# Kernel tuning notes

Hardware: AMD Instinct MI355X
Metric: run time of the kernel (lower is better)

The kernel has to match this reference:

```python
import jax, jax.numpy as jnp
import numpy as np

BN_EPS = 1e-5


def setup_inputs() -> dict:
    key = jax.random.key(0)
    ks = jax.random.split(key, 6)
    N, C, T, V = 64, 64, 300, 25
    num_A, O = 3, 64
    x = jax.random.normal(ks[0], (N, C, T, V), dtype=jnp.float32)
    A = jax.random.uniform(ks[1], (num_A, V, V), dtype=jnp.float32)
    # 1x1 conv weights per adjacency branch: W[a, o, c], bias b[a, o]
    W = jax.random.normal(ks[2], (num_A, O, C), dtype=jnp.float32) * (1.0 / np.sqrt(C))
    b = jax.random.normal(ks[3], (num_A, O), dtype=jnp.float32) * 0.01
    gamma = jnp.ones((O,), dtype=jnp.float32)
    beta = jnp.zeros((O,), dtype=jnp.float32)
    return {"x": x, "A": A, "W": W, "b": b, "gamma": gamma, "beta": beta}


def reference(x, A, W, b, gamma, beta):
    # x: [N, C, T, V]; A: [num_A, V, V]; W: [num_A, O, C]; b: [num_A, O]
    # For each branch a: xa = x @ A_a over the joint dim V, then a 1x1 conv
    # (channel mix W_a + bias b_a), accumulated over branches.
    z = jnp.einsum('nctv,avw->anctw', x, A)          # [num_A, N, C, T, V]
    y = jnp.einsum('anctw,aoc->notw', z, W)          # [N, O, T, V]
    y = y + jnp.sum(b, axis=0)[None, :, None, None]
    # BatchNorm2d (training mode: batch statistics over N, T, V per channel)
    mean = jnp.mean(y, axis=(0, 2, 3), keepdims=True)
    var = jnp.mean((y - mean) ** 2, axis=(0, 2, 3), keepdims=True)
    y = (y - mean) * jax.lax.rsqrt(var + BN_EPS)
    y = y * gamma[None, :, None, None] + beta[None, :, None, None]
    return jax.nn.relu(y)
```

## Files before the change

### kernel.cpp

```cpp
#include <hip/hip_runtime.h>


typedef __attribute__((ext_vector_type(8))) short short8;
typedef __attribute__((ext_vector_type(4))) float f32x4;

static __device__ __forceinline__ float bf2f(unsigned short u) {
    return __uint_as_float(((unsigned)u) << 16);
}
static __device__ __forceinline__ unsigned short f2bf(float f) {
    unsigned u = __float_as_uint(f);
    u += 0x7FFFu + ((u >> 16) & 1u);
    return (unsigned short)(u >> 16);
}

#define MFMA16(a, b, c) __builtin_amdgcn_mfma_f32_16x16x32_bf16((a), (b), (c), 0, 0, 0)

__global__ __launch_bounds__(256, 4)
void gcn_k1(const void* __restrict__ xg, const void* __restrict__ Ag,
            const void* __restrict__ Wg, const void* __restrict__ gammag,
            float* __restrict__ gstats, unsigned short* __restrict__ y_ws)
{
    const int tid  = threadIdx.x;
    const int wv   = tid >> 6;
    const int lane = tid & 63;
    const int n16  = lane & 15;
    const int kg   = lane >> 4;
    const int bx   = blockIdx.x;
    const int nb   = bx / 75;
    const int tile = bx - nb * 75;

    const bool isbf = (*(const unsigned*)gammag) == 0x3F803F80u;

    __shared__ __align__(16) unsigned short xs2[256 * 32];
    __shared__ __align__(16) unsigned short AsT[3 * 32 * 32];
    __shared__ __align__(16) unsigned short zsT[112 * 68];
    __shared__ float red[128];

    if (tid < 128) red[tid] = 0.f;

    short8 wfrag[3][2];
    #pragma unroll
    for (int a = 0; a < 3; ++a)
        #pragma unroll
        for (int k2 = 0; k2 < 2; ++k2) {
            const int off = (a * 64 + wv * 16 + n16) * 64 + k2 * 32 + kg * 8;
            if (isbf) {
                wfrag[a][k2] = *(const short8*)((const unsigned short*)Wg + off);
            } else {
                const float* wp = (const float*)Wg + off;
                const float4 w0 = *(const float4*)wp;
                const float4 w1 = *(const float4*)(wp + 4);
                short8 f;
                f[0] = (short)f2bf(w0.x); f[1] = (short)f2bf(w0.y);
                f[2] = (short)f2bf(w0.z); f[3] = (short)f2bf(w0.w);
                f[4] = (short)f2bf(w1.x); f[5] = (short)f2bf(w1.y);
                f[6] = (short)f2bf(w1.z); f[7] = (short)f2bf(w1.w);
                wfrag[a][k2] = f;
            }
        }

    for (int s = tid; s < 3072; s += 256) {
        const int a = s >> 10, w = (s >> 5) & 31, v = s & 31;
        unsigned short val = 0;
        if (v < 25 && w < 25) {
            const int src = (a * 25 + v) * 25 + w;
            val = isbf ? ((const unsigned short*)Ag)[src] : f2bf(((const float*)Ag)[src]);
        }
        AsT[s] = val;
    }

    {
        #pragma unroll
        for (int vv = 25; vv < 32; ++vv) xs2[tid * 32 + vv] = 0;
    }
    if (isbf) {
        const unsigned* xp = (const unsigned*)xg;
        for (int p = tid; p < 3200; p += 256) {
            const int c = p / 50, pc = p - c * 50;
            const unsigned u = xp[(nb * 64 + c) * 3750 + tile * 50 + pc];
            const int r0 = pc * 2, r1 = r0 + 1;
            const int dt0 = r0 / 25, v0 = r0 - dt0 * 25;
            const int dt1 = r1 / 25, v1 = r1 - dt1 * 25;
            xs2[(c * 4 + dt0) * 32 + v0] = (unsigned short)(u & 0xFFFFu);
            xs2[(c * 4 + dt1) * 32 + v1] = (unsigned short)(u >> 16);
        }
    } else {
        const float2* xp = (const float2*)xg;
        for (int p = tid; p < 3200; p += 256) {
            const int c = p / 50, pc = p - c * 50;
            const float2 f = xp[(nb * 64 + c) * 3750 + tile * 50 + pc];
            const int r0 = pc * 2, r1 = r0 + 1;
            const int dt0 = r0 / 25, v0 = r0 - dt0 * 25;
            const int dt1 = r1 / 25, v1 = r1 - dt1 * 25;
            xs2[(c * 4 + dt0) * 32 + v0] = f2bf(f.x);
            xs2[(c * 4 + dt1) * 32 + v1] = f2bf(f.y);
        }
    }

    __syncthreads();

    f32x4 acc[7];
    #pragma unroll
    for (int mt = 0; mt < 7; ++mt) acc[mt] = (f32x4){0.f, 0.f, 0.f, 0.f};

    const f32x4 zero4 = (f32x4){0.f, 0.f, 0.f, 0.f};

    #pragma unroll
    for (int a = 0; a < 3; ++a) {
        const short8 bA0 = *(const short8*)&AsT[(a * 32 +      n16) * 32 + kg * 8];
        const short8 bA1 = *(const short8*)&AsT[(a * 32 + 16 + n16) * 32 + kg * 8];
        f32x4 d[4][2];
        #pragma unroll
        for (int mt = 0; mt < 4; ++mt) {
            const short8 af = *(const short8*)&xs2[(wv * 64 + mt * 16 + n16) * 32 + kg * 8];
            d[mt][0] = MFMA16(af, bA0, zero4);
            d[mt][1] = MFMA16(af, bA1, zero4);
        }
        #pragma unroll
        for (int mt = 0; mt < 4; ++mt) {
            const int c = 16 * wv + mt * 4 + kg;
            #pragma unroll
            for (int r = 0; r < 4; ++r) {
                const int w0 = n16;
                zsT[(r * 25 + w0) * 68 + c] = f2bf(d[mt][0][r]);
                const int w1 = 16 + n16;
                if (w1 < 25) zsT[(r * 25 + w1) * 68 + c] = f2bf(d[mt][1][r]);
            }
        }
        __syncthreads();

        #pragma unroll
        for (int mt = 0; mt < 7; ++mt) {
            #pragma unroll
            for (int k2 = 0; k2 < 2; ++k2) {
                const unsigned short* zp = &zsT[(mt * 16 + n16) * 68 + k2 * 32 + kg * 8];
                const ushort4 z0 = *(const ushort4*)zp;
                const ushort4 z1 = *(const ushort4*)(zp + 4);
                short8 bf;
                bf[0] = (short)z0.x; bf[1] = (short)z0.y; bf[2] = (short)z0.z; bf[3] = (short)z0.w;
                bf[4] = (short)z1.x; bf[5] = (short)z1.y; bf[6] = (short)z1.z; bf[7] = (short)z1.w;
                acc[mt] = MFMA16(wfrag[a][k2], bf, acc[mt]);
            }
        }
        __syncthreads();
    }

    #pragma unroll
    for (int r = 0; r < 4; ++r) {
        const int o = 16 * wv + kg * 4 + r;
        const unsigned rowbase = (unsigned)(nb * 64 + o) * 7500u + (unsigned)tile * 100u;
        float s = 0.f, q = 0.f;
        #pragma unroll
        for (int mt = 0; mt < 7; ++mt) {
            const float v = acc[mt][r];
            const bool valid = (mt < 6) | (n16 < 4);
            const float vm = valid ? v : 0.f;
            s += vm; q += vm * vm;
            const float vhi = __shfl_xor(v, 1);
            if (((n16 & 1) == 0) && valid) {
                const unsigned idx = rowbase + (unsigned)(mt * 16 + n16);
                *(unsigned*)(y_ws + idx) = (unsigned)f2bf(v) | ((unsigned)f2bf(vhi) << 16);
            }
        }
        #pragma unroll
        for (int off = 1; off < 16; off <<= 1) {
            s += __shfl_xor(s, off);
            q += __shfl_xor(q, off);
        }
        if (n16 == 0) { atomicAdd(&red[o], s); atomicAdd(&red[64 + o], q); }
    }

    __syncthreads();
    if (tid < 128) atomicAdd(&gstats[tid], red[tid]);
}

__global__ __launch_bounds__(256)
void gcn_k2(const float* __restrict__ gstats, const unsigned* __restrict__ y32,
            const void* __restrict__ gammag, const void* __restrict__ betag,
            void* __restrict__ outg)
{
    __shared__ float sc[64], sh[64];
    const int tid = threadIdx.x;
    const bool isbf = (*(const unsigned*)gammag) == 0x3F803F80u;

    if (tid < 64) {
        const float inv  = 1.0f / 480000.0f;
        const float mean = gstats[tid] * inv;
        const float var  = gstats[64 + tid] * inv - mean * mean;
        const float rstd = rsqrtf(var + 1e-5f);
        float g, be;
        if (isbf) { g = bf2f(((const unsigned short*)gammag)[tid]); be = bf2f(((const unsigned short*)betag)[tid]); }
        else      { g = ((const float*)gammag)[tid];                be = ((const float*)betag)[tid]; }
        sc[tid] = g * rstd;
        sh[tid] = be - mean * g * rstd;
    }
    __syncthreads();

    const unsigned i = blockIdx.x * 256u + (unsigned)tid;
    const uint4 u = ((const uint4*)y32)[i];
    const unsigned b = i * 4u;
    unsigned wv[4] = {u.x, u.y, u.z, u.w};
    float res[8];
    #pragma unroll
    for (int j = 0; j < 4; ++j) {
        const unsigned o = ((b + j) / 3750u) & 63u;
        const float scl = sc[o], shf = sh[o];
        const float v0 = bf2f((unsigned short)(wv[j] & 0xFFFFu));
        const float v1 = bf2f((unsigned short)(wv[j] >> 16));
        res[2 * j]     = fmaxf(fmaf(v0, scl, shf), 0.f);
        res[2 * j + 1] = fmaxf(fmaf(v1, scl, shf), 0.f);
    }
    if (isbf) {
        uint4 outp;
        outp.x = (unsigned)f2bf(res[0]) | ((unsigned)f2bf(res[1]) << 16);
        outp.y = (unsigned)f2bf(res[2]) | ((unsigned)f2bf(res[3]) << 16);
        outp.z = (unsigned)f2bf(res[4]) | ((unsigned)f2bf(res[5]) << 16);
        outp.w = (unsigned)f2bf(res[6]) | ((unsigned)f2bf(res[7]) << 16);
        ((uint4*)outg)[i] = outp;
    } else {
        float4 f0 = make_float4(res[0], res[1], res[2], res[3]);
        float4 f1 = make_float4(res[4], res[5], res[6], res[7]);
        ((float4*)outg)[2 * i]     = f0;
        ((float4*)outg)[2 * i + 1] = f1;
    }
}

extern "C" void kernel_launch(void* const* d_in, const int* in_sizes, int n_in,
                              void* d_out, int out_size, void* d_ws, size_t ws_size,
                              hipStream_t stream)
{
    (void)in_sizes; (void)n_in; (void)out_size; (void)ws_size;
    const void* x     = d_in[0];
    const void* A     = d_in[1];
    const void* W     = d_in[2];
    const void* gamma = d_in[4];
    const void* beta  = d_in[5];

    float*          gstats = (float*)d_ws;
    unsigned short* y_ws   = (unsigned short*)d_ws + 256;

    hipMemsetAsync(d_ws, 0, 512, stream);
    gcn_k1<<<dim3(64 * 75), dim3(256), 0, stream>>>(x, A, W, gamma, gstats, y_ws);
    gcn_k2<<<dim3(15000), dim3(256), 0, stream>>>(gstats, (const unsigned*)y_ws, gamma, beta, d_out);
}
```

Before: 382.0 us.

## Recompute GEMMs in a second pass instead of storing intermediate y

Replaces the store-y-then-normalize scheme with a templated kernel run twice: the first pass computes only BatchNorm statistics, and the second recomputes the graph conv and channel mix and writes the normalized ReLU output directly. This removes the write and re-read of the bf16 intermediate tensor. In exchange x is read twice and all the MFMA work is done twice. Tiles grow to 12 timesteps per block, each wave keeps its z tile in its own swizzled LDS buffer with no block barriers, and W fragments are loaded per branch.

```diff
diff --git a/kernel.cpp b/kernel.cpp
--- a/kernel.cpp
+++ b/kernel.cpp
@@ -1,4 +1,5 @@
 #include <hip/hip_runtime.h>
+#include <hip/hip_bf16.h>
 
 
 typedef __attribute__((ext_vector_type(8))) short short8;
@@ -12,13 +13,27 @@
     u += 0x7FFFu + ((u >> 16) & 1u);
     return (unsigned short)(u >> 16);
 }
+static __device__ __forceinline__ unsigned pk2(float lo, float hi) {
+    return (unsigned)f2bf(lo) | ((unsigned)f2bf(hi) << 16);
+}
+static __device__ __forceinline__ short8 cvt8(float4 a, float4 b) {
+    short8 r;
+    r[0] = (short)f2bf(a.x); r[1] = (short)f2bf(a.y);
+    r[2] = (short)f2bf(a.z); r[3] = (short)f2bf(a.w);
+    r[4] = (short)f2bf(b.x); r[5] = (short)f2bf(b.y);
+    r[6] = (short)f2bf(b.z); r[7] = (short)f2bf(b.w);
+    return r;
+}
 
 #define MFMA16(a, b, c) __builtin_amdgcn_mfma_f32_16x16x32_bf16((a), (b), (c), 0, 0, 0)
-
-__global__ __launch_bounds__(256, 4)
-void gcn_k1(const void* __restrict__ xg, const void* __restrict__ Ag,
-            const void* __restrict__ Wg, const void* __restrict__ gammag,
-            float* __restrict__ gstats, unsigned short* __restrict__ y_ws)
+#define LDS_FENCE() __asm__ volatile("s_waitcnt lgkmcnt(0)" ::: "memory")
+
+template <bool STORE>
+__global__ __launch_bounds__(256, 2)
+void gcn_core(const void* __restrict__ xg, const void* __restrict__ Ag,
+              const void* __restrict__ Wg, const void* __restrict__ gammag,
+              const void* __restrict__ betag, float* __restrict__ gstats,
+              void* __restrict__ outg)
 {
     const int tid  = threadIdx.x;
     const int wv   = tid >> 6;
@@ -26,39 +41,63 @@
     const int n16  = lane & 15;
     const int kg   = lane >> 4;
     const int bx   = blockIdx.x;
-    const int nb   = bx / 75;
-    const int tile = bx - nb * 75;
+    const int nb   = bx / 25;
+    const int tile = bx - nb * 25;
+    const int t0   = tile * 12 + wv * 3;
 
     const bool isbf = (*(const unsigned*)gammag) == 0x3F803F80u;
 
-    __shared__ __align__(16) unsigned short xs2[256 * 32];
+    __shared__ __align__(16) unsigned short xls[768 * 32];
+    __shared__ __align__(16) unsigned short zbuf[4 * 2048];
     __shared__ __align__(16) unsigned short AsT[3 * 32 * 32];
-    __shared__ __align__(16) unsigned short zsT[112 * 68];
     __shared__ float red[128];
-
-    if (tid < 128) red[tid] = 0.f;
-
-    short8 wfrag[3][2];
-    #pragma unroll
-    for (int a = 0; a < 3; ++a)
-        #pragma unroll
-        for (int k2 = 0; k2 < 2; ++k2) {
-            const int off = (a * 64 + wv * 16 + n16) * 64 + k2 * 32 + kg * 8;
-            if (isbf) {
-                wfrag[a][k2] = *(const short8*)((const unsigned short*)Wg + off);
-            } else {
-                const float* wp = (const float*)Wg + off;
-                const float4 w0 = *(const float4*)wp;
-                const float4 w1 = *(const float4*)(wp + 4);
-                short8 f;
-                f[0] = (short)f2bf(w0.x); f[1] = (short)f2bf(w0.y);
-                f[2] = (short)f2bf(w0.z); f[3] = (short)f2bf(w0.w);
-                f[4] = (short)f2bf(w1.x); f[5] = (short)f2bf(w1.y);
-                f[6] = (short)f2bf(w1.z); f[7] = (short)f2bf(w1.w);
-                wfrag[a][k2] = f;
-            }
-        }
-
+    __shared__ float scsh[128];
+
+    if (!STORE) {
+        if (tid < 128) red[tid] = 0.f;
+    } else {
+        if (tid < 64) {
+            const float inv  = 1.0f / 480000.0f;
+            const float mean = gstats[tid] * inv;
+            const float var  = gstats[64 + tid] * inv - mean * mean;
+            const float rstd = rsqrtf(var + 1e-5f);
+            float g, be;
+            if (isbf) { g = bf2f(((const unsigned short*)gammag)[tid]); be = bf2f(((const unsigned short*)betag)[tid]); }
+            else      { g = ((const float*)gammag)[tid];                be = ((const float*)betag)[tid]; }
+            scsh[tid]      = g * rstd;
+            scsh[64 + tid] = be - mean * g * rstd;
+        }
+    }
+
+    for (int p = tid; p < 5376; p += 256) {
+        const int row = p / 7, v = 25 + (p - 7 * row);
+        xls[row * 32 + v] = 0;
+    }
+    if (isbf) {
+        const unsigned* xp = (const unsigned*)xg;
+        const unsigned cb = (unsigned)(nb * 64) * 3750u + (unsigned)tile * 150u;
+        for (int p = tid; p < 9600; p += 256) {
+            const int c = p / 150, r = p - 150 * c;
+            const unsigned u = xp[cb + (unsigned)c * 3750u + r];
+            const int e = 2 * r;
+            const int t1 = e / 25,      v1 = e - 25 * t1;
+            const int t2 = (e + 1) / 25, v2 = (e + 1) - 25 * t2;
+            xls[(t1 * 64 + c) * 32 + v1] = (unsigned short)(u & 0xFFFFu);
+            xls[(t2 * 64 + c) * 32 + v2] = (unsigned short)(u >> 16);
+        }
+    } else {
+        const float2* xp = (const float2*)xg;
+        const unsigned cb = (unsigned)(nb * 64) * 3750u + (unsigned)tile * 150u;
+        for (int p = tid; p < 9600; p += 256) {
+            const int c = p / 150, r = p - 150 * c;
+            const float2 f = xp[cb + (unsigned)c * 3750u + r];
+            const int e = 2 * r;
+            const int t1 = e / 25,      v1 = e - 25 * t1;
+            const int t2 = (e + 1) / 25, v2 = (e + 1) - 25 * t2;
+            xls[(t1 * 64 + c) * 32 + v1] = f2bf(f.x);
+            xls[(t2 * 64 + c) * 32 + v2] = f2bf(f.y);
+        }
+    }
     for (int s = tid; s < 3072; s += 256) {
         const int a = s >> 10, w = (s >> 5) & 31, v = s & 31;
         unsigned short val = 0;
@@ -69,159 +108,154 @@
         AsT[s] = val;
     }
 
-    {
-        #pragma unroll
-        for (int vv = 25; vv < 32; ++vv) xs2[tid * 32 + vv] = 0;
-    }
-    if (isbf) {
-        const unsigned* xp = (const unsigned*)xg;
-        for (int p = tid; p < 3200; p += 256) {
-            const int c = p / 50, pc = p - c * 50;
-            const unsigned u = xp[(nb * 64 + c) * 3750 + tile * 50 + pc];
-            const int r0 = pc * 2, r1 = r0 + 1;
-            const int dt0 = r0 / 25, v0 = r0 - dt0 * 25;
-            const int dt1 = r1 / 25, v1 = r1 - dt1 * 25;
-            xs2[(c * 4 + dt0) * 32 + v0] = (unsigned short)(u & 0xFFFFu);
-            xs2[(c * 4 + dt1) * 32 + v1] = (unsigned short)(u >> 16);
-        }
-    } else {
-        const float2* xp = (const float2*)xg;
-        for (int p = tid; p < 3200; p += 256) {
-            const int c = p / 50, pc = p - c * 50;
-            const float2 f = xp[(nb * 64 + c) * 3750 + tile * 50 + pc];
-            const int r0 = pc * 2, r1 = r0 + 1;
-            const int dt0 = r0 / 25, v0 = r0 - dt0 * 25;
-            const int dt1 = r1 / 25, v1 = r1 - dt1 * 25;
-            xs2[(c * 4 + dt0) * 32 + v0] = f2bf(f.x);
-            xs2[(c * 4 + dt1) * 32 + v1] = f2bf(f.y);
-        }
-    }
-
     __syncthreads();
 
-    f32x4 acc[7];
+    short8 xf[3][4];
     #pragma unroll
-    for (int mt = 0; mt < 7; ++mt) acc[mt] = (f32x4){0.f, 0.f, 0.f, 0.f};
+    for (int dt = 0; dt < 3; ++dt)
+        #pragma unroll
+        for (int ct = 0; ct < 4; ++ct)
+            xf[dt][ct] = *(const short8*)&xls[((wv * 3 + dt) * 64 + 16 * ct + n16) * 32 + 8 * kg];
+
+    f32x4 acc[3][2][4];
+    #pragma unroll
+    for (int dt = 0; dt < 3; ++dt)
+        #pragma unroll
+        for (int wt = 0; wt < 2; ++wt)
+            #pragma unroll
+            for (int ot = 0; ot < 4; ++ot)
+                acc[dt][wt][ot] = (f32x4){0.f, 0.f, 0.f, 0.f};
 
     const f32x4 zero4 = (f32x4){0.f, 0.f, 0.f, 0.f};
+    unsigned short* zb = &zbuf[wv * 2048];
+    const int swz = n16 & 7;
 
     #pragma unroll
     for (int a = 0; a < 3; ++a) {
-        const short8 bA0 = *(const short8*)&AsT[(a * 32 +      n16) * 32 + kg * 8];
-        const short8 bA1 = *(const short8*)&AsT[(a * 32 + 16 + n16) * 32 + kg * 8];
-        f32x4 d[4][2];
-        #pragma unroll
-        for (int mt = 0; mt < 4; ++mt) {
-            const short8 af = *(const short8*)&xs2[(wv * 64 + mt * 16 + n16) * 32 + kg * 8];
-            d[mt][0] = MFMA16(af, bA0, zero4);
-            d[mt][1] = MFMA16(af, bA1, zero4);
-        }
-        #pragma unroll
-        for (int mt = 0; mt < 4; ++mt) {
-            const int c = 16 * wv + mt * 4 + kg;
-            #pragma unroll
-            for (int r = 0; r < 4; ++r) {
-                const int w0 = n16;
-                zsT[(r * 25 + w0) * 68 + c] = f2bf(d[mt][0][r]);
-                const int w1 = 16 + n16;
-                if (w1 < 25) zsT[(r * 25 + w1) * 68 + c] = f2bf(d[mt][1][r]);
+        short8 wf[4][2];
+        #pragma unroll
+        for (int ot = 0; ot < 4; ++ot)
+            #pragma unroll
+            for (int h = 0; h < 2; ++h) {
+                const int off = ((a * 64 + 16 * ot + n16) * 64 + 32 * h + 8 * kg);
+                if (isbf) {
+                    wf[ot][h] = *(const short8*)((const unsigned short*)Wg + off);
+                } else {
+                    const float* wp = (const float*)Wg + off;
+                    wf[ot][h] = cvt8(*(const float4*)wp, *(const float4*)(wp + 4));
+                }
+            }
+        const short8 af0 = *(const short8*)&AsT[(a * 32 +      n16) * 32 + 8 * kg];
+        const short8 af1 = *(const short8*)&AsT[(a * 32 + 16 + n16) * 32 + 8 * kg];
+
+        #pragma unroll
+        for (int dt = 0; dt < 3; ++dt) {
+            LDS_FENCE();
+            #pragma unroll
+            for (int ct = 0; ct < 4; ++ct) {
+                const f32x4 d0 = MFMA16(xf[dt][ct], af0, zero4);
+                const f32x4 d1 = MFMA16(xf[dt][ct], af1, zero4);
+                const int gp = (2 * ct + (kg >> 1)) ^ swz;
+                const int so = gp * 8 + (kg & 1) * 4;
+                {   unsigned* p = (unsigned*)(zb + n16 * 64 + so);
+                    p[0] = pk2(d0[0], d0[1]); p[1] = pk2(d0[2], d0[3]); }
+                {   unsigned* p = (unsigned*)(zb + (16 + n16) * 64 + so);
+                    p[0] = pk2(d1[0], d1[1]); p[1] = pk2(d1[2], d1[3]); }
+            }
+            LDS_FENCE();
+            #pragma unroll
+            for (int wt = 0; wt < 2; ++wt)
+                #pragma unroll
+                for (int h = 0; h < 2; ++h) {
+                    const int gp = (4 * h + kg) ^ swz;
+                    const short8 zf = *(const short8*)(zb + (16 * wt + n16) * 64 + gp * 8);
+                    #pragma unroll
+                    for (int ot = 0; ot < 4; ++ot)
+                        acc[dt][wt][ot] = MFMA16(zf, wf[ot][h], acc[dt][wt][ot]);
+                }
+        }
+    }
+
+    if (!STORE) {
+        float s[4], q[4];
+        #pragma unroll
+        for (int ot = 0; ot < 4; ++ot) { s[ot] = 0.f; q[ot] = 0.f; }
+        #pragma unroll
+        for (int dt = 0; dt < 3; ++dt)
+            #pragma unroll
+            for (int wt = 0; wt < 2; ++wt)
+                #pragma unroll
+                for (int ot = 0; ot < 4; ++ot)
+                    #pragma unroll
+                    for (int r = 0; r < 4; ++r) {
+                        const float v = acc[dt][wt][ot][r];
+                        s[ot] += v; q[ot] += v * v;
+                    }
+        #pragma unroll
+        for (int ot = 0; ot < 4; ++ot) {
+            s[ot] += __shfl_xor(s[ot], 16); s[ot] += __shfl_xor(s[ot], 32);
+            q[ot] += __shfl_xor(q[ot], 16); q[ot] += __shfl_xor(q[ot], 32);
+        }
+        if (kg == 0) {
+            #pragma unroll
+            for (int ot = 0; ot < 4; ++ot) {
+                atomicAdd(&red[16 * ot + n16], s[ot]);
+                atomicAdd(&red[64 + 16 * ot + n16], q[ot]);
             }
         }
         __syncthreads();
-
-        #pragma unroll
-        for (int mt = 0; mt < 7; ++mt) {
-            #pragma unroll
-            for (int k2 = 0; k2 < 2; ++k2) {
-                const unsigned short* zp = &zsT[(mt * 16 + n16) * 68 + k2 * 32 + kg * 8];
-                const ushort4 z0 = *(const ushort4*)zp;
-                const ushort4 z1 = *(const ushort4*)(zp + 4);
-                short8 bf;
-                bf[0] = (short)z0.x; bf[1] = (short)z0.y; bf[2] = (short)z0.z; bf[3] = (short)z0.w;
-                bf[4] = (short)z1.x; bf[5] = (short)z1.y; bf[6] = (short)z1.z; bf[7] = (short)z1.w;
-                acc[mt] = MFMA16(wfrag[a][k2], bf, acc[mt]);
-            }
-        }
-        __syncthreads();
-    }
-
-    #pragma unroll
-    for (int r = 0; r < 4; ++r) {
-        const int o = 16 * wv + kg * 4 + r;
-        const unsigned rowbase = (unsigned)(nb * 64 + o) * 7500u + (unsigned)tile * 100u;
-        float s = 0.f, q = 0.f;
-        #pragma unroll
-        for (int mt = 0; mt < 7; ++mt) {
-            const float v = acc[mt][r];
-            const bool valid = (mt < 6) | (n16 < 4);
-            const float vm = valid ? v : 0.f;
-            s += vm; q += vm * vm;
-            const float vhi = __shfl_xor(v, 1);
-            if (((n16 & 1) == 0) && valid) {
-                const unsigned idx = rowbase + (unsigned)(mt * 16 + n16);
-                *(unsigned*)(y_ws + idx) = (unsigned)f2bf(v) | ((unsigned)f2bf(vhi) << 16);
-            }
-        }
-        #pragma unroll
-        for (int off = 1; off < 16; off <<= 1) {
-            s += __shfl_xor(s, off);
-            q += __shfl_xor(q, off);
-        }
-        if (n16 == 0) { atomicAdd(&red[o], s); atomicAdd(&red[64 + o], q); }
-    }
-
-    __syncthreads();
-    if (tid < 128) atomicAdd(&gstats[tid], red[tid]);
-}
-
-__global__ __launch_bounds__(256)
-void gcn_k2(const float* __restrict__ gstats, const unsigned* __restrict__ y32,
-            const void* __restrict__ gammag, const void* __restrict__ betag,
-            void* __restrict__ outg)
-{
-    __shared__ float sc[64], sh[64];
-    const int tid = threadIdx.x;
-    const bool isbf = (*(const unsigned*)gammag) == 0x3F803F80u;
-
-    if (tid < 64) {
-        const float inv  = 1.0f / 480000.0f;
-        const float mean = gstats[tid] * inv;
-        const float var  = gstats[64 + tid] * inv - mean * mean;
-        const float rstd = rsqrtf(var + 1e-5f);
-        float g, be;
-        if (isbf) { g = bf2f(((const unsigned short*)gammag)[tid]); be = bf2f(((const unsigned short*)betag)[tid]); }
-        else      { g = ((const float*)gammag)[tid];                be = ((const float*)betag)[tid]; }
-        sc[tid] = g * rstd;
-        sh[tid] = be - mean * g * rstd;
-    }
-    __syncthreads();
-
-    const unsigned i = blockIdx.x * 256u + (unsigned)tid;
-    const uint4 u = ((const uint4*)y32)[i];
-    const unsigned b = i * 4u;
-    unsigned wv[4] = {u.x, u.y, u.z, u.w};
-    float res[8];
-    #pragma unroll
-    for (int j = 0; j < 4; ++j) {
-        const unsigned o = ((b + j) / 3750u) & 63u;
-        const float scl = sc[o], shf = sh[o];
-        const float v0 = bf2f((unsigned short)(wv[j] & 0xFFFFu));
-        const float v1 = bf2f((unsigned short)(wv[j] >> 16));
-        res[2 * j]     = fmaxf(fmaf(v0, scl, shf), 0.f);
-        res[2 * j + 1] = fmaxf(fmaf(v1, scl, shf), 0.f);
-    }
-    if (isbf) {
-        uint4 outp;
-        outp.x = (unsigned)f2bf(res[0]) | ((unsigned)f2bf(res[1]) << 16);
-        outp.y = (unsigned)f2bf(res[2]) | ((unsigned)f2bf(res[3]) << 16);
-        outp.z = (unsigned)f2bf(res[4]) | ((unsigned)f2bf(res[5]) << 16);
-        outp.w = (unsigned)f2bf(res[6]) | ((unsigned)f2bf(res[7]) << 16);
-        ((uint4*)outg)[i] = outp;
+        if (tid < 128) atomicAdd(&gstats[tid], red[tid]);
     } else {
-        float4 f0 = make_float4(res[0], res[1], res[2], res[3]);
-        float4 f1 = make_float4(res[4], res[5], res[6], res[7]);
-        ((float4*)outg)[2 * i]     = f0;
-        ((float4*)outg)[2 * i + 1] = f1;
+        float scl[4], shf[4];
+        #pragma unroll
+        for (int ot = 0; ot < 4; ++ot) {
+            scl[ot] = scsh[16 * ot + n16];
+            shf[ot] = scsh[64 + 16 * ot + n16];
+        }
+        #pragma unroll
+        for (int dt = 0; dt < 3; ++dt) {
+            const int t = t0 + dt;
+            const bool teven = ((t & 1) == 0);
+            #pragma unroll
+            for (int ot = 0; ot < 4; ++ot) {
+                const int o = 16 * ot + n16;
+                const unsigned rowbase = ((unsigned)(nb * 64 + o) * 300u + (unsigned)t) * 25u;
+                #pragma unroll
+                for (int wt = 0; wt < 2; ++wt) {
+                    if (wt == 1 && kg == 3) continue;
+                    const float v0 = fmaxf(fmaf(acc[dt][wt][ot][0], scl[ot], shf[ot]), 0.f);
+                    const float v1 = fmaxf(fmaf(acc[dt][wt][ot][1], scl[ot], shf[ot]), 0.f);
+                    const float v2 = fmaxf(fmaf(acc[dt][wt][ot][2], scl[ot], shf[ot]), 0.f);
+                    const float v3 = fmaxf(fmaf(acc[dt][wt][ot][3], scl[ot], shf[ot]), 0.f);
+                    const unsigned e = rowbase + (unsigned)(16 * wt + 4 * kg);
+                    if (isbf) {
+                        unsigned short* op = (unsigned short*)outg;
+                        if (wt == 1 && kg == 2) {
+                            op[e] = f2bf(v0);
+                        } else if (teven) {
+                            *(unsigned*)(op + e)     = pk2(v0, v1);
+                            *(unsigned*)(op + e + 2) = pk2(v2, v3);
+                        } else {
+                            op[e] = f2bf(v0);
+                            *(unsigned*)(op + e + 1) = pk2(v1, v2);
+                            op[e + 3] = f2bf(v3);
+                        }
+                    } else {
+                        float* op = (float*)outg;
+                        if (wt == 1 && kg == 2) {
+                            op[e] = v0;
+                        } else if (teven) {
+                            *(float2*)(op + e)     = make_float2(v0, v1);
+                            *(float2*)(op + e + 2) = make_float2(v2, v3);
+                        } else {
+                            op[e] = v0;
+                            *(float2*)(op + e + 1) = make_float2(v1, v2);
+                            op[e + 3] = v3;
+                        }
+                    }
+                }
+            }
+        }
     }
 }
 
@@ -236,10 +270,9 @@
     const void* gamma = d_in[4];
     const void* beta  = d_in[5];
 
-    float*          gstats = (float*)d_ws;
-    unsigned short* y_ws   = (unsigned short*)d_ws + 256;
+    float* gstats = (float*)d_ws;
 
     hipMemsetAsync(d_ws, 0, 512, stream);
-    gcn_k1<<<dim3(64 * 75), dim3(256), 0, stream>>>(x, A, W, gamma, gstats, y_ws);
-    gcn_k2<<<dim3(15000), dim3(256), 0, stream>>>(gstats, (const unsigned*)y_ws, gamma, beta, d_out);
-}
+    gcn_core<false><<<dim3(1600), dim3(256), 0, stream>>>(x, A, W, gamma, beta, gstats, d_out);
+    gcn_core<true ><<<dim3(1600), dim3(256), 0, stream>>>(x, A, W, gamma, beta, gstats, d_out);
+}
```

Result: slower. 499.9 us (+30.9%).
